# Optimization experiments

Hardware: AMD Instinct MI355X
Metric: run time of the kernel (lower is better)

## Reference

```python
import jax, jax.numpy as jnp
import numpy as np

B, L, D = 256, 512, 512

def setup_inputs() -> dict:
    key = jax.random.key(0)
    k1, k2, k3, k4, k5 = jax.random.split(key, 5)
    scale = 1.0 / np.sqrt(D)  # keep logits in a sane range
    return {
        "text_features": jax.random.normal(k1, (B, L, D), dtype=jnp.float32),
        "image_features": jax.random.normal(k2, (B, D), dtype=jnp.float32),
        "W_ML": jax.random.normal(k3, (D, D), dtype=jnp.float32) * scale,
        "W_MV": jax.random.normal(k4, (D, D), dtype=jnp.float32) * scale,
        "tau": jnp.ones((1,), dtype=jnp.float32),
        "padding_mask": jax.random.randint(k5, (B, L), 0, 2).astype(bool),
    }

def reference(text_features, image_features, W_ML, W_MV, tau, padding_mask):
    b, l, _ = text_features.shape
    tau_c = jnp.clip(tau, 0.001)  # [1]
    valid = ~padding_mask  # [B,L] True where token is real
    # Linear(bias=False): y = x @ W.T
    text_proj = jnp.einsum('bld,ed->ble', text_features, W_ML)   # [B,L,D]
    image_proj = jnp.einsum('bd,ed->be', image_features, W_MV)   # [B,D]
    neg_inf = jnp.float32(-jnp.inf)
    # positive scores: own image vs own text tokens
    s_iji = jnp.einsum('bd,bld->bl', image_proj, text_proj) / tau_c  # [B,L]
    # all-images-vs-text denominator: s_kji[i,l,k] = <text[i,l], image[k]>
    s_kji = jnp.einsum('ild,kd->ilk', text_proj, image_proj) / tau_c  # [B,L,B]
    mask_kj = valid.T[None, :, :]  # [1,L,B] -> valid[k,l] per (i,l,k)
    s_kji = jnp.where(mask_kj, s_kji, neg_inf)
    denom_log = jax.nn.logsumexp(s_kji, axis=2)  # [B,L]
    # cross-batch text negatives: s_iok[i,k,l] = <image[i], text[k,l]>
    s_iok = jnp.einsum('id,kld->ikl', image_proj, text_proj) / tau_c  # [B,B,L]
    mask_ko = valid[None, :, :]  # [1,B,L]
    mask_neq = ~jnp.eye(b, dtype=bool)[:, :, None]  # exclude k == i
    s_iok_f = jnp.where(mask_ko & mask_neq, s_iok, neg_inf).reshape(b, -1)
    cross_log = jax.nn.logsumexp(s_iok_f, axis=1)  # [B]
    neg_log = jnp.logaddexp(s_iji, cross_log[:, None])  # [B,L]
    denom_log = jnp.where(valid, denom_log, 0.0)
    neg_log = jnp.where(valid, neg_log, 0.0)
    f1 = denom_log - s_iji
    f2 = neg_log - s_iji
    loss_mat = 0.5 * (f1 + f2)
    n_valid = jnp.sum(valid)
    loss = jnp.sum(jnp.where(valid, loss_mat, 0.0)) / n_valid
    return loss
```

## Files before the change

kernel.cpp:

```cpp
#include <hip/hip_runtime.h>
#include <math.h>


#define B_ 256
#define L_ 512
#define D_ 512
#define ROWS (B_ * L_)
#define NT (ROWS / 64)
#define NEG_INF (-INFINITY)

typedef __attribute__((ext_vector_type(8))) short s8_t;
typedef __attribute__((ext_vector_type(4))) float f4_t;
typedef __attribute__((ext_vector_type(2))) float f2_t;
typedef __attribute__((ext_vector_type(4))) unsigned short us4_t;

typedef __attribute__((address_space(3))) unsigned int lds_u32;
typedef const __attribute__((address_space(1))) unsigned int glb_u32;

__device__ inline unsigned short f2bf(float x) {
    unsigned int u = __float_as_uint(x);
    u += 0x7FFFu + ((u >> 16) & 1u);
    return (unsigned short)(u >> 16);
}

__global__ __launch_bounds__(256) void ip_kernel(const float* __restrict__ img,
                                                 const float* __restrict__ Wmv,
                                                 float* __restrict__ ip) {
    int kt = blockIdx.x >> 3, et = blockIdx.x & 7;
    __shared__ float Ast[32][36];
    __shared__ float Bst[32][72];
    int tid = threadIdx.x;
    int ty = tid >> 4;
    int tx = tid & 15;
    float acc[2][4] = {};
    int sr = tid >> 3, sc = (tid & 7) * 4;
    for (int d0 = 0; d0 < D_; d0 += 32) {
        f4_t a = *(const f4_t*)(img + (size_t)(kt * 32 + sr) * D_ + d0 + sc);
        f4_t b0 = *(const f4_t*)(Wmv + (size_t)(et * 64 + sr) * D_ + d0 + sc);
        f4_t b1 = *(const f4_t*)(Wmv + (size_t)(et * 64 + sr + 32) * D_ + d0 + sc);
        __syncthreads();
#pragma unroll
        for (int m = 0; m < 4; m++) {
            Ast[sc + m][sr] = a[m];
            Bst[sc + m][sr] = b0[m];
            Bst[sc + m][sr + 32] = b1[m];
        }
        __syncthreads();
#pragma unroll 4
        for (int d = 0; d < 32; d++) {
            f2_t a2 = *(const f2_t*)&Ast[d][ty * 2];
            f4_t b4 = *(const f4_t*)&Bst[d][tx * 4];
#pragma unroll
            for (int i = 0; i < 2; i++)
#pragma unroll
                for (int j = 0; j < 4; j++) acc[i][j] = fmaf(a2[i], b4[j], acc[i][j]);
        }
    }
#pragma unroll
    for (int i = 0; i < 2; i++) {
        f4_t o; o[0] = acc[i][0]; o[1] = acc[i][1]; o[2] = acc[i][2]; o[3] = acc[i][3];
        *(f4_t*)(ip + (size_t)(kt * 32 + ty * 2 + i) * D_ + et * 64 + tx * 4) = o;
    }
}

__global__ __launch_bounds__(256) void c_kernel(const float* __restrict__ ip,
                                                const float* __restrict__ Wml,
                                                const float* __restrict__ tau,
                                                unsigned short* __restrict__ Cb2) {
    int kt = blockIdx.x >> 3, dt = blockIdx.x & 7;
    __shared__ float Ast[32][36];
    __shared__ float Bst[32][72];
    int tid = threadIdx.x;
    int ty = tid >> 4;
    int tx = tid & 15;
    float acc[2][4] = {};
    int sr = tid >> 3, sc = (tid & 7) * 4;
    int br = tid >> 4, bc = (tid & 15) * 4;
    for (int e0 = 0; e0 < D_; e0 += 32) {
        f4_t a = *(const f4_t*)(ip + (size_t)(kt * 32 + sr) * D_ + e0 + sc);
        f4_t b0 = *(const f4_t*)(Wml + (size_t)(e0 + br) * D_ + dt * 64 + bc);
        f4_t b1 = *(const f4_t*)(Wml + (size_t)(e0 + br + 16) * D_ + dt * 64 + bc);
        __syncthreads();
#pragma unroll
        for (int m = 0; m < 4; m++) Ast[sc + m][sr] = a[m];
        *(f4_t*)&Bst[br][bc] = b0;
        *(f4_t*)&Bst[br + 16][bc] = b1;
        __syncthreads();
#pragma unroll 4
        for (int e = 0; e < 32; e++) {
            f2_t a2 = *(const f2_t*)&Ast[e][ty * 2];
            f4_t b4 = *(const f4_t*)&Bst[e][tx * 4];
#pragma unroll
            for (int i = 0; i < 2; i++)
#pragma unroll
                for (int j = 0; j < 4; j++) acc[i][j] = fmaf(a2[i], b4[j], acc[i][j]);
        }
    }
    float it = 1.0f / fmaxf(tau[0], 0.001f);
#pragma unroll
    for (int i = 0; i < 2; i++) {
        us4_t o;
#pragma unroll
        for (int j = 0; j < 4; j++) o[j] = f2bf(acc[i][j] * it);
        int n = kt * 32 + ty * 2 + i;
        int kk0 = dt * 64 + tx * 4;
        *(us4_t*)(Cb2 + (size_t)((kk0 >> 3) * 256 + n) * 8 + (kk0 & 7)) = o;
    }
}

__global__ __launch_bounds__(256) void mask_kernel(const int* __restrict__ pad,
                                                   unsigned long long* __restrict__ mbits) {
    int l = blockIdx.x;
    int w = threadIdx.x >> 6;
    int j = threadIdx.x & 63;
    unsigned long long bal = __ballot(pad[(w * 64 + j) * L_ + l] == 0);
    if (j == 0) mbits[l * 4 + w] = bal;
}

#define ACC(mt, nt, r) ((mt) ? acc1[nt][r] : acc0[nt][r])

#define MERGE_XOR(m, s, msk) do {                                        \
        float mo_ = __shfl_xor(m, msk);                                  \
        float so_ = __shfl_xor(s, msk);                                  \
        float M_ = fmaxf(m, mo_);                                        \
        s = (M_ > NEG_INF) ? (s * __expf(m - M_) + so_ * __expf(mo_ - M_)) : 0.f; \
        m = M_;                                                          \
    } while (0)

__global__ __launch_bounds__(256, 3) void gemm_mfma_kernel(
    const float* __restrict__ text, const unsigned short* __restrict__ Cb2,
    const unsigned long long* __restrict__ mbits,
    float* __restrict__ denom, float* __restrict__ siji,
    float* __restrict__ crossM, float* __restrict__ crossS) {
    __shared__ __align__(16) unsigned char smem[32768];

    const int tile = blockIdx.x;
    const int row0 = tile * 64;
    const int bIdx = row0 >> 9;
    const int l0 = row0 & 511;
    const int tid = threadIdx.x;
    const int wave = tid >> 6;
    const int lane = tid & 63;
    const int qd = lane >> 4;
    const int mm = lane & 15;
    const int wr = wave >> 1;
    const int wc = wave & 1;

    f4_t acc0[8], acc1[8];
#pragma unroll
    for (int nt = 0; nt < 8; nt++)
#pragma unroll
        for (int r = 0; r < 4; r++) { acc0[nt][r] = 0.f; acc1[nt][r] = 0.f; }

    const float* aRow = text + (size_t)(row0 + wr * 32 + mm) * D_ + qd * 8;

    f4_t ar[4];
#define LOAD_A(t) do { \
        ar[0] = *(const f4_t*)(aRow + (t) * 32); \
        ar[1] = *(const f4_t*)(aRow + (t) * 32 + 4); \
        ar[2] = *(const f4_t*)(aRow + 16 * D_ + (t) * 32); \
        ar[3] = *(const f4_t*)(aRow + 16 * D_ + (t) * 32 + 4); \
    } while (0)

#define STAGE(buf, t) do { \
        const unsigned char* gsrc_ = (const unsigned char*)Cb2 + (size_t)(t) * 16384 + wave * 1024 + lane * 16; \
        unsigned char* ldst_ = smem + (buf) * 16384 + wave * 1024; \
        _Pragma("unroll") \
        for (int i_ = 0; i_ < 4; i_++) \
            __builtin_amdgcn_global_load_lds((glb_u32*)(gsrc_ + i_ * 4096), \
                                             (lds_u32*)(ldst_ + i_ * 4096), 16, 0, 0); \
    } while (0)

    STAGE(0, 0);
    LOAD_A(0);
    int cur = 0;
#pragma unroll 1
    for (int t = 0; t < 16; t++) {
        __syncthreads();
        if (t < 15) STAGE(cur ^ 1, t + 1);
        s8_t aa0, aa1;
#pragma unroll
        for (int j = 0; j < 4; j++) {
            aa0[j] = (short)f2bf(ar[0][j]); aa0[j + 4] = (short)f2bf(ar[1][j]);
            aa1[j] = (short)f2bf(ar[2][j]); aa1[j + 4] = (short)f2bf(ar[3][j]);
        }
        if (t < 15) LOAD_A(t + 1);
        const unsigned short* bbase =
            (const unsigned short*)(smem + cur * 16384) + qd * 2048 + (wc * 128 + mm) * 8;
#pragma unroll
        for (int nt = 0; nt < 8; nt++) {
            s8_t bf = *(const s8_t*)(bbase + nt * 128);
            acc0[nt] = __builtin_amdgcn_mfma_f32_16x16x32_bf16(aa0, bf, acc0[nt], 0, 0, 0);
            acc1[nt] = __builtin_amdgcn_mfma_f32_16x16x32_bf16(aa1, bf, acc1[nt], 0, 0, 0);
        }
        cur ^= 1;
    }
    __syncthreads();

    float* fp  = (float*)smem;
    float* pmp = fp;
    float* psp = fp + 128;
    float* cmp = fp + 256;
    float* csp = fp + 768;

    const int mw = bIdx >> 6, mb = bIdx & 63;

    float radj[2][4];
#pragma unroll
    for (int mt = 0; mt < 2; mt++)
#pragma unroll
        for (int r = 0; r < 4; r++) {
            int l = l0 + wr * 32 + mt * 16 + qd * 4 + r;
            radj[mt][r] = ((mbits[l * 4 + mw] >> mb) & 1ULL) ? 0.f : NEG_INF;
        }

#pragma unroll
    for (int nt = 0; nt < 8; nt++) {
        float m = NEG_INF;
#pragma unroll
        for (int mt = 0; mt < 2; mt++)
#pragma unroll
            for (int r = 0; r < 4; r++) m = fmaxf(m, ACC(mt, nt, r) + radj[mt][r]);
        float s = 0.f;
        if (m > NEG_INF) {
#pragma unroll
            for (int mt = 0; mt < 2; mt++)
#pragma unroll
                for (int r = 0; r < 4; r++) s += __expf(ACC(mt, nt, r) + radj[mt][r] - m);
        }
        MERGE_XOR(m, s, 16);
        MERGE_XOR(m, s, 32);
        if (qd == 0) {
            int col = wc * 128 + nt * 16 + mm;
            cmp[wr * 256 + col] = m;
            csp[wr * 256 + col] = s;
        }
    }

#pragma unroll
    for (int mt = 0; mt < 2; mt++)
#pragma unroll
        for (int r = 0; r < 4; r++) {
            int rl = wr * 32 + mt * 16 + qd * 4 + r;
            int l = l0 + rl;
            unsigned long long w0 = mbits[l * 4 + wc * 2] >> mm;
            unsigned long long w1 = mbits[l * 4 + wc * 2 + 1] >> mm;
            float v[8];
#pragma unroll
            for (int nt = 0; nt < 4; nt++) {
                v[nt]     = ACC(mt, nt, r)     + (((w0 >> (nt * 16)) & 1ULL) ? 0.f : NEG_INF);
                v[nt + 4] = ((mt) ? acc1[nt + 4][r] : acc0[nt + 4][r])
                            + (((w1 >> (nt * 16)) & 1ULL) ? 0.f : NEG_INF);
            }
            float m = NEG_INF;
#pragma unroll
            for (int nt = 0; nt < 8; nt++) m = fmaxf(m, v[nt]);
            float s = 0.f;
            if (m > NEG_INF) {
#pragma unroll
                for (int nt = 0; nt < 8; nt++) s += __expf(v[nt] - m);
            }
            MERGE_XOR(m, s, 1);
            MERGE_XOR(m, s, 2);
            MERGE_XOR(m, s, 4);
            MERGE_XOR(m, s, 8);
            if (mm == 0) { pmp[wc * 64 + rl] = m; psp[wc * 64 + rl] = s; }
        }

#pragma unroll
    for (int nt = 0; nt < 8; nt++)
        if (wc == (bIdx >> 7) && mm == (bIdx & 15) && nt == ((bIdx >> 4) & 7)) {
#pragma unroll
            for (int mt = 0; mt < 2; mt++)
#pragma unroll
                for (int r = 0; r < 4; r++)
                    siji[row0 + wr * 32 + mt * 16 + qd * 4 + r] = ACC(mt, nt, r);
        }

    __syncthreads();

    if (tid < 64) {
        float m0 = pmp[tid], m1 = pmp[64 + tid];
        float s0 = psp[tid], s1 = psp[64 + tid];
        float M = fmaxf(m0, m1);
        float dl = NEG_INF;
        if (M > NEG_INF) dl = M + __logf(s0 * __expf(m0 - M) + s1 * __expf(m1 - M));
        denom[row0 + tid] = dl;
    }
    {
        int col = tid;
        float m0 = cmp[col], m1 = cmp[256 + col];
        float s0 = csp[col], s1 = csp[256 + col];
        float M = fmaxf(m0, m1);
        float s = (M > NEG_INF) ? (s0 * __expf(m0 - M) + s1 * __expf(m1 - M)) : 0.f;
        if (col == bIdx) { M = NEG_INF; s = 0.f; }
        crossM[(size_t)col * NT + tile] = M;
        crossS[(size_t)col * NT + tile] = s;
    }
#undef LOAD_A
#undef STAGE
}

__global__ __launch_bounds__(256) void cross_combine_kernel(const float* __restrict__ crossM,
                                                            const float* __restrict__ crossS,
                                                            float* __restrict__ crossLog) {
    int i = blockIdx.x;
    int tid = threadIdx.x;
    float m = NEG_INF, s = 0.f;
    for (int e = 0; e < NT / 256; e++) {
        int t = e * 256 + tid;
        float m2 = crossM[(size_t)i * NT + t];
        float s2 = crossS[(size_t)i * NT + t];
        if (m2 > NEG_INF) {
            if (m == NEG_INF) { m = m2; s = s2; }
            else {
                float M = fmaxf(m, m2);
                s = s * expf(m - M) + s2 * expf(m2 - M);
                m = M;
            }
        }
    }
    __shared__ float sm[256], ss[256];
    sm[tid] = m; ss[tid] = s;
    __syncthreads();
    for (int off = 128; off > 0; off >>= 1) {
        if (tid < off) {
            float m1 = sm[tid], s1 = ss[tid];
            float m2 = sm[tid + off], s2 = ss[tid + off];
            float M = fmaxf(m1, m2);
            float sv;
            if (M == NEG_INF) sv = 0.f;
            else sv = s1 * expf(m1 - M) + s2 * expf(m2 - M);
            sm[tid] = M; ss[tid] = sv;
        }
        __syncthreads();
    }
    if (tid == 0) crossLog[i] = (sm[0] == NEG_INF) ? NEG_INF : sm[0] + logf(ss[0]);
}

__global__ __launch_bounds__(256) void loss_partial_kernel(
    const int* __restrict__ pad, const float* __restrict__ denom,
    const float* __restrict__ siji, const float* __restrict__ crossLog,
    float* __restrict__ psum, float* __restrict__ pcnt) {
    int tid = threadIdx.x;
    int idx = blockIdx.x * 256 + tid;
    float term = 0.f, cnt = 0.f;
    if (pad[idx] == 0) {
        float dl = denom[idx], sv = siji[idx], cl = crossLog[idx >> 9];
        float M = fmaxf(sv, cl);
        float neg = M + log1pf(expf(-fabsf(sv - cl)));
        term = 0.5f * (dl + neg) - sv;
        cnt = 1.f;
    }
    __shared__ float bs[256], bc[256];
    bs[tid] = term; bc[tid] = cnt;
    __syncthreads();
    for (int off = 128; off > 0; off >>= 1) {
        if (tid < off) { bs[tid] += bs[tid + off]; bc[tid] += bc[tid + off]; }
        __syncthreads();
    }
    if (tid == 0) { psum[blockIdx.x] = bs[0]; pcnt[blockIdx.x] = bc[0]; }
}

__global__ __launch_bounds__(256) void final_kernel(const float* __restrict__ psum,
                                                    const float* __restrict__ pcnt,
                                                    float* __restrict__ out) {
    int tid = threadIdx.x;
    __shared__ float bs[256], bc[256];
    bs[tid] = psum[tid] + psum[tid + 256];
    bc[tid] = pcnt[tid] + pcnt[tid + 256];
    __syncthreads();
    for (int off = 128; off > 0; off >>= 1) {
        if (tid < off) { bs[tid] += bs[tid + off]; bc[tid] += bc[tid + off]; }
        __syncthreads();
    }
    if (tid == 0) out[0] = bs[0] / bc[0];
}

extern "C" void kernel_launch(void* const* d_in, const int* in_sizes, int n_in,
                              void* d_out, int out_size, void* d_ws, size_t ws_size,
                              hipStream_t stream) {
    (void)in_sizes; (void)n_in; (void)out_size; (void)ws_size;
    const float* text = (const float*)d_in[0];
    const float* img  = (const float*)d_in[1];
    const float* Wml  = (const float*)d_in[2];
    const float* Wmv  = (const float*)d_in[3];
    const float* tau  = (const float*)d_in[4];
    const int* pad    = (const int*)d_in[5];
    float* out = (float*)d_out;

    float* ws = (float*)d_ws;
    float* ip       = ws;
    unsigned short* Cb2 = (unsigned short*)(ws + 131072);
    unsigned long long* mbits = (unsigned long long*)(ws + 262144);
    float* denom    = ws + 266240;
    float* siji     = ws + 397312;
    float* crossM   = ws + 528384;
    float* crossS   = ws + 1052672;
    float* crossLog = ws + 1576960;
    float* psum     = ws + 1577216;
    float* pcnt     = ws + 1577728;

    hipLaunchKernelGGL(ip_kernel,   dim3(64),  dim3(256), 0, stream, img, Wmv, ip);
    hipLaunchKernelGGL(c_kernel,    dim3(64),  dim3(256), 0, stream, ip, Wml, tau, Cb2);
    hipLaunchKernelGGL(mask_kernel, dim3(L_),  dim3(256), 0, stream, pad, mbits);
    hipLaunchKernelGGL(gemm_mfma_kernel, dim3(NT), dim3(256), 0, stream,
                       text, Cb2, mbits, denom, siji, crossM, crossS);
    hipLaunchKernelGGL(cross_combine_kernel, dim3(B_), dim3(256), 0, stream,
                       crossM, crossS, crossLog);
    hipLaunchKernelGGL(loss_partial_kernel, dim3(ROWS / 256), dim3(256), 0, stream,
                       pad, denom, siji, crossLog, psum, pcnt);
    hipLaunchKernelGGL(final_kernel, dim3(1), dim3(256), 0, stream, psum, pcnt, out);
}
```

Before: 462.2 us.

## Deepen A-register prefetch to two stages with explicit waitcnt barriers

Restructures the GEMM main loop into a manually unrolled two-iteration body. The A operand is prefetched two K-steps ahead into alternating register sets, and sched_barrier plus explicit s_waitcnt vmcnt/s_barrier replace __syncthreads so loads can stay in flight across the barrier. It also raises the launch-bounds occupancy hint from 3 to 4 blocks per CU. The extra register set raises register pressure, and the higher occupancy target may force spills. The hand-written vmcnt counts must match the exact load issue order or the LDS data will be read early.

```diff
diff --git a/kernel.cpp b/kernel.cpp
--- a/kernel.cpp
+++ b/kernel.cpp
@@ -127,7 +127,7 @@
         m = M_;                                                          \
     } while (0)
 
-__global__ __launch_bounds__(256, 3) void gemm_mfma_kernel(
+__global__ __launch_bounds__(256, 4) void gemm_mfma_kernel(
     const float* __restrict__ text, const unsigned short* __restrict__ Cb2,
     const unsigned long long* __restrict__ mbits,
     float* __restrict__ denom, float* __restrict__ siji,
@@ -154,12 +154,12 @@
 
     const float* aRow = text + (size_t)(row0 + wr * 32 + mm) * D_ + qd * 8;
 
-    f4_t ar[4];
-#define LOAD_A(t) do { \
-        ar[0] = *(const f4_t*)(aRow + (t) * 32); \
-        ar[1] = *(const f4_t*)(aRow + (t) * 32 + 4); \
-        ar[2] = *(const f4_t*)(aRow + 16 * D_ + (t) * 32); \
-        ar[3] = *(const f4_t*)(aRow + 16 * D_ + (t) * 32 + 4); \
+    f4_t ar0[4], ar1[4];
+#define LOAD_A(dst, t) do { \
+        dst[0] = *(const f4_t*)(aRow + (t) * 32); \
+        dst[1] = *(const f4_t*)(aRow + (t) * 32 + 4); \
+        dst[2] = *(const f4_t*)(aRow + 16 * D_ + (t) * 32); \
+        dst[3] = *(const f4_t*)(aRow + 16 * D_ + (t) * 32 + 4); \
     } while (0)
 
 #define STAGE(buf, t) do { \
@@ -171,29 +171,63 @@
                                              (lds_u32*)(ldst_ + i_ * 4096), 16, 0, 0); \
     } while (0)
 
+#define CVT(arc, aa0, aa1) do { \
+        _Pragma("unroll") \
+        for (int j_ = 0; j_ < 4; j_++) { \
+            aa0[j_] = (short)f2bf(arc[0][j_]); aa0[j_ + 4] = (short)f2bf(arc[1][j_]); \
+            aa1[j_] = (short)f2bf(arc[2][j_]); aa1[j_ + 4] = (short)f2bf(arc[3][j_]); \
+        } \
+    } while (0)
+
+#define MFMA8(rb, aa0, aa1) do { \
+        const unsigned short* bbase_ = \
+            (const unsigned short*)(smem + (rb) * 16384) + qd * 2048 + (wc * 128 + mm) * 8; \
+        _Pragma("unroll") \
+        for (int nt_ = 0; nt_ < 8; nt_++) { \
+            s8_t bf_ = *(const s8_t*)(bbase_ + nt_ * 128); \
+            acc0[nt_] = __builtin_amdgcn_mfma_f32_16x16x32_bf16(aa0, bf_, acc0[nt_], 0, 0, 0); \
+            acc1[nt_] = __builtin_amdgcn_mfma_f32_16x16x32_bf16(aa1, bf_, acc1[nt_], 0, 0, 0); \
+        } \
+    } while (0)
+
+#define ITER(tt, rb, sb, arc) do { \
+        STAGE(sb, (tt) + 1); \
+        __builtin_amdgcn_sched_barrier(0); \
+        s8_t aa0_, aa1_; \
+        CVT(arc, aa0_, aa1_); \
+        LOAD_A(arc, (tt) + 2); \
+        __builtin_amdgcn_sched_barrier(0); \
+        MFMA8(rb, aa0_, aa1_); \
+        asm volatile("s_waitcnt vmcnt(4)" ::: "memory"); \
+        __builtin_amdgcn_s_barrier(); \
+    } while (0)
+
     STAGE(0, 0);
-    LOAD_A(0);
-    int cur = 0;
+    __builtin_amdgcn_sched_barrier(0);
+    LOAD_A(ar0, 0);
+    LOAD_A(ar1, 1);
+    __builtin_amdgcn_sched_barrier(0);
+    asm volatile("s_waitcnt vmcnt(8)" ::: "memory");
+    __builtin_amdgcn_s_barrier();
+
 #pragma unroll 1
-    for (int t = 0; t < 16; t++) {
-        __syncthreads();
-        if (t < 15) STAGE(cur ^ 1, t + 1);
-        s8_t aa0, aa1;
-#pragma unroll
-        for (int j = 0; j < 4; j++) {
-            aa0[j] = (short)f2bf(ar[0][j]); aa0[j + 4] = (short)f2bf(ar[1][j]);
-            aa1[j] = (short)f2bf(ar[2][j]); aa1[j + 4] = (short)f2bf(ar[3][j]);
-        }
-        if (t < 15) LOAD_A(t + 1);
-        const unsigned short* bbase =
-            (const unsigned short*)(smem + cur * 16384) + qd * 2048 + (wc * 128 + mm) * 8;
-#pragma unroll
-        for (int nt = 0; nt < 8; nt++) {
-            s8_t bf = *(const s8_t*)(bbase + nt * 128);
-            acc0[nt] = __builtin_amdgcn_mfma_f32_16x16x32_bf16(aa0, bf, acc0[nt], 0, 0, 0);
-            acc1[nt] = __builtin_amdgcn_mfma_f32_16x16x32_bf16(aa1, bf, acc1[nt], 0, 0, 0);
-        }
-        cur ^= 1;
+    for (int t = 0; t < 14; t += 2) {
+        ITER(t,     0, 1, ar0);
+        ITER(t + 1, 1, 0, ar1);
+    }
+    {
+        STAGE(1, 15);
+        __builtin_amdgcn_sched_barrier(0);
+        s8_t aa0_, aa1_;
+        CVT(ar0, aa0_, aa1_);
+        MFMA8(0, aa0_, aa1_);
+        asm volatile("s_waitcnt vmcnt(0)" ::: "memory");
+        __builtin_amdgcn_s_barrier();
+    }
+    {
+        s8_t aa0_, aa1_;
+        CVT(ar1, aa0_, aa1_);
+        MFMA8(1, aa0_, aa1_);
     }
     __syncthreads();
 
@@ -299,6 +333,9 @@
     }
 #undef LOAD_A
 #undef STAGE
+#undef CVT
+#undef MFMA8
+#undef ITER
 }
 
 __global__ __launch_bounds__(256) void cross_combine_kernel(const float* __restrict__ crossM,
```

New measurement: 463.0 us. About the same (+0.2%).
